# Performance work log

Measured on AMD Instinct MI355X. Metric: run time of the kernel, lower is better.

The kernel has to match this reference:

```python
import jax, jax.numpy as jnp
import numpy as np

N = 100000
E = 1600000
F_FEAT, F_COND, F_HID, F_LAT = 128, 32, 128, 64


def setup_inputs() -> dict:
    key = jax.random.key(0)
    ks = jax.random.split(key, 16)
    feature = jax.random.normal(ks[0], (N, F_FEAT), dtype=jnp.float32)
    condition = jax.random.normal(ks[1], (N, F_COND), dtype=jnp.float32)
    edge_index = jax.random.randint(ks[2], (2, E), 0, N, dtype=jnp.int64)

    def glorot(k, fan_in, fan_out):
        s = jnp.sqrt(6.0 / (fan_in + fan_out)).astype(jnp.float32)
        return jax.random.uniform(k, (fan_in, fan_out), jnp.float32, -s, s)

    enc_in = F_FEAT + F_COND   # 160
    dec_in = F_LAT + F_COND    # 96
    return {
        "feature": feature,
        "condition": condition,
        "edge_index": edge_index,
        "W_e1": glorot(ks[3], enc_in, F_HID), "b_e1": jnp.zeros((F_HID,), jnp.float32),
        "W_e2": glorot(ks[4], F_HID, F_HID), "b_e2": jnp.zeros((F_HID,), jnp.float32),
        "W_e3": glorot(ks[5], F_HID, F_LAT), "b_e3": jnp.zeros((F_LAT,), jnp.float32),
        "W_d1": glorot(ks[6], dec_in, F_HID), "b_d1": jnp.zeros((F_HID,), jnp.float32),
        "W_d2": glorot(ks[7], F_HID, F_HID), "b_d2": jnp.zeros((F_HID,), jnp.float32),
        "W_d3": glorot(ks[8], F_HID, F_FEAT), "b_d3": jnp.zeros((F_FEAT,), jnp.float32),
    }


def _gcn_conv(x, W, b, src, dst, dinv):
    # GCNConv with add_self_loops=True, symmetric normalization:
    # out = D^{-1/2} (A + I) D^{-1/2} X W + b
    h = x @ W                                        # [N, out]
    coef = (dinv[src] * dinv[dst])[:, None]          # [E, 1]
    msg = h[src] * coef                              # [E, out]
    agg = jax.ops.segment_sum(msg, dst, num_segments=x.shape[0])
    agg = agg + h * (dinv * dinv)[:, None]           # self-loop term
    return agg + b


def reference(feature, condition, edge_index,
              W_e1, b_e1, W_e2, b_e2, W_e3, b_e3,
              W_d1, b_d1, W_d2, b_d2, W_d3, b_d3):
    src, dst = edge_index[0], edge_index[1]
    n = feature.shape[0]
    # degree with self loops (edge weights = 1)
    deg = jax.ops.segment_sum(jnp.ones((src.shape[0],), jnp.float32), dst,
                              num_segments=n) + 1.0
    dinv = jax.lax.rsqrt(deg)

    # encoder
    x = jnp.concatenate([feature, condition], axis=1)
    h = jnp.tanh(_gcn_conv(x, W_e1, b_e1, src, dst, dinv))
    h = jnp.tanh(_gcn_conv(h, W_e2, b_e2, src, dst, dinv))
    z = _gcn_conv(h, W_e3, b_e3, src, dst, dinv)

    # decoder
    x = jnp.concatenate([z, condition], axis=1)
    h = jnp.tanh(_gcn_conv(x, W_d1, b_d1, src, dst, dinv))
    h = jnp.tanh(_gcn_conv(h, W_d2, b_d2, src, dst, dinv))
    out = _gcn_conv(h, W_d3, b_d3, src, dst, dinv)
    return out
```

## Files before the change

kernel.cpp:

```cpp
#include <hip/hip_runtime.h>
#include <hip/hip_fp16.h>
#include <math.h>

#define NN 100000
#define NE 1600000
#define NB ((NN + 255) >> 8)
#define CHUNK 8192
#define CAP 8192

typedef __attribute__((ext_vector_type(4))) float floatx4;
typedef __attribute__((ext_vector_type(8))) short shortx8;


__global__ __launch_bounds__(256)
void coarse_hist(const int* __restrict__ ei, int* __restrict__ bucket_cnt, int E) {
    __shared__ int h[512];
    int t = threadIdx.x;
    for (int i = t; i < 512; i += 256) h[i] = 0;
    __syncthreads();
    int base = blockIdx.x * CHUNK;
    int lim = min(base + CHUNK, E);
    for (int e = base + t; e < lim; e += 256) {
        int d = ei[E + e];
        atomicAdd(&h[d >> 8], 1);
    }
    __syncthreads();
    for (int i = t; i < 512; i += 256)
        if (h[i]) atomicAdd(&bucket_cnt[i], h[i]);
}

__global__ void scan_buckets(const int* __restrict__ bucket_cnt,
                             int* __restrict__ bucket_base,
                             int* __restrict__ bucket_fill) {
    __shared__ int sh[512];
    int t = threadIdx.x;
    int v = (t < NB) ? bucket_cnt[t] : 0;
    sh[t] = v;
    __syncthreads();
    for (int off = 1; off < 512; off <<= 1) {
        int u = (t >= off) ? sh[t - off] : 0;
        __syncthreads();
        sh[t] += u;
        __syncthreads();
    }
    int ex = (t == 0) ? 0 : sh[t - 1];
    if (t <= NB) bucket_base[t] = ex;
    if (t < NB) bucket_fill[t] = ex;
}

__global__ __launch_bounds__(256)
void coarse_scatter(const int* __restrict__ ei, int* __restrict__ bucket_fill,
                    unsigned long long* __restrict__ pairs, int E) {
    __shared__ int h[512];
    __shared__ int base[512];
    int t = threadIdx.x;
    for (int i = t; i < 512; i += 256) h[i] = 0;
    __syncthreads();
    int cbase = blockIdx.x * CHUNK;
    int lim = min(cbase + CHUNK, E);
    for (int e = cbase + t; e < lim; e += 256) {
        int d = ei[E + e];
        atomicAdd(&h[d >> 8], 1);
    }
    __syncthreads();
    for (int i = t; i < 512; i += 256)
        base[i] = h[i] ? atomicAdd(&bucket_fill[i], h[i]) : 0;
    __syncthreads();
    for (int i = t; i < 512; i += 256) h[i] = 0;
    __syncthreads();
    for (int e = cbase + t; e < lim; e += 256) {
        int s = ei[e];
        int d = ei[E + e];
        int b = d >> 8;
        int r = atomicAdd(&h[b], 1);
        pairs[base[b] + r] =
            ((unsigned long long)(unsigned)d << 32) | (unsigned)s;
    }
}

__global__ __launch_bounds__(256)
void fine_csr(const unsigned long long* __restrict__ pairs,
              const int* __restrict__ bucket_base,
              int* __restrict__ rowptr, int* __restrict__ colid,
              float* __restrict__ dinv, int n) {
    __shared__ int hist[256];
    __shared__ int offs[256];
    __shared__ int rank[256];
    __shared__ int lbuf[CAP];
    int b = blockIdx.x, t = threadIdx.x;
    int beg = bucket_base[b], end = bucket_base[b + 1];
    int cnt = end - beg;
    hist[t] = 0; rank[t] = 0;
    __syncthreads();
    for (int i = t; i < cnt; i += 256) {
        int d = (int)(pairs[beg + i] >> 32);
        atomicAdd(&hist[d & 255], 1);
    }
    __syncthreads();
    int v = hist[t];
    offs[t] = v;
    __syncthreads();
    for (int off = 1; off < 256; off <<= 1) {
        int u = (t >= off) ? offs[t - off] : 0;
        __syncthreads();
        offs[t] += u;
        __syncthreads();
    }
    int ex = (t == 0) ? 0 : offs[t - 1];
    int node = (b << 8) + t;
    if (node < n) {
        rowptr[node] = beg + ex;
        dinv[node] = rsqrtf((float)v + 1.0f);
    } else if (node == n) {
        rowptr[n] = beg + ex;
    }
    __syncthreads();
    offs[t] = ex;
    __syncthreads();
    for (int i = t; i < cnt; i += 256) {
        unsigned long long p = pairs[beg + i];
        int d = (int)(p >> 32) & 255;
        int s = (int)(p & 0xffffffffu);
        int r = atomicAdd(&rank[d], 1);
        lbuf[offs[d] + r] = s;
    }
    __syncthreads();
    for (int i = t; i < cnt; i += 256) colid[beg + i] = lbuf[i];
}


__device__ __forceinline__ void wsplit_one(const float* __restrict__ W,
                                           unsigned short* __restrict__ Wsw,
                                           int i, int K, int OUT) {
    int k = i / OUT, o = i % OUT;
    float w = W[i];
    unsigned u = __float_as_uint(w);
    float r = w - __uint_as_float(u & 0xFFFF0000u);
    int NT = OUT >> 4;
    int ktc = k >> 5, q = (k >> 3) & 3, j = k & 7;
    int nt = o >> 4, mm = o & 15;
    int lane = (q << 4) | mm;
    size_t base = ((((size_t)(ktc * NT + nt) * 2) * 64 + lane) << 3) + j;
    Wsw[base] = (unsigned short)(u >> 16);
    Wsw[base + 512] = (unsigned short)(__float_as_uint(r) >> 16);
}

__global__ __launch_bounds__(256)
void wsplit_all(const float* __restrict__ W0, unsigned short* __restrict__ O0,
                const float* __restrict__ W1, unsigned short* __restrict__ O1,
                const float* __restrict__ W2, unsigned short* __restrict__ O2,
                const float* __restrict__ W3, unsigned short* __restrict__ O3,
                const float* __restrict__ W4, unsigned short* __restrict__ O4,
                const float* __restrict__ W5, unsigned short* __restrict__ O5) {
    int i = blockIdx.x * 256 + threadIdx.x;
    if (i < 20480) { wsplit_one(W0, O0, i, 160, 128); return; }
    i -= 20480;
    if (i < 16384) { wsplit_one(W1, O1, i, 128, 128); return; }
    i -= 16384;
    if (i < 8192)  { wsplit_one(W2, O2, i, 128, 64);  return; }
    i -= 8192;
    if (i < 12288) { wsplit_one(W3, O3, i, 96, 128);  return; }
    i -= 12288;
    if (i < 16384) { wsplit_one(W4, O4, i, 128, 128); return; }
    i -= 16384;
    if (i < 16384) { wsplit_one(W5, O5, i, 128, 128); }
}


__device__ __forceinline__ void split8(const float* v, shortx8& hi, shortx8& lo) {
#pragma unroll
    for (int i = 0; i < 8; i++) {
        unsigned u = __float_as_uint(v[i]);
        float r = v[i] - __uint_as_float(u & 0xFFFF0000u);
        hi[i] = (short)(u >> 16);
        lo[i] = (short)(__float_as_uint(r) >> 16);
    }
}

template <int OUT, int K, int K1>
__global__ __launch_bounds__(512, 4)
void gemm_mfma(const float* __restrict__ X1, const float* __restrict__ X2,
               const unsigned short* __restrict__ Wsw,
               const float* __restrict__ dinv,
               __half* __restrict__ Y, int ntiles) {
    constexpr int NT = OUT / 16;
    constexpr int NKTC = K / 32;
    constexpr int K2 = K - K1;
    constexpr int PERC = OUT * 128;
    constexpr int CSZ = (65536 / PERC < NKTC) ? (65536 / PERC) : NKTC;
    __shared__ __align__(16) unsigned short lds[CSZ * PERC / 2];

    const int t = threadIdx.x;
    const int wave = t >> 6, lane = t & 63;
    const int m = lane & 15, q = lane >> 4;
    const int tile0 = blockIdx.x * 16 + wave * 2;
    const int tile1 = tile0 + 1;
    const bool act0 = tile0 < ntiles;
    const bool act1 = tile1 < ntiles;
    const int r0 = act0 ? tile0 * 16 + m : 0;
    const int r1 = act1 ? tile1 * 16 + m : 0;
    const float* ap1a = X1 + (size_t)r0 * K1 + q * 8;
    const float* ap1b = X1 + (size_t)r1 * K1 + q * 8;
    const float* ap2a = (K2 > 0) ? (X2 + (size_t)r0 * K2 + q * 8) : X1;
    const float* ap2b = (K2 > 0) ? (X2 + (size_t)r1 * K2 + q * 8) : X1;

    floatx4 acc0[NT], acc1[NT];
#pragma unroll
    for (int nt = 0; nt < NT; nt++) {
        acc0[nt] = (floatx4){0.f, 0.f, 0.f, 0.f};
        acc1[nt] = (floatx4){0.f, 0.f, 0.f, 0.f};
    }

#pragma unroll
    for (int c0 = 0; c0 < NKTC; c0 += CSZ) {
        const int cl = (NKTC - c0 < CSZ) ? (NKTC - c0) : CSZ;
        if (c0 != 0) __syncthreads();
        {
            const float4* gs = (const float4*)Wsw + (size_t)c0 * (PERC / 16);
            float4* ld = (float4*)lds;
            int tot = cl * (PERC / 16);
            for (int i = t; i < tot; i += 512) ld[i] = gs[i];
        }
        __syncthreads();
#pragma unroll
        for (int ktc = 0; ktc < cl; ktc++) {
            const int kg = (c0 + ktc) * 32;
            const float* pa = (kg < K1) ? (ap1a + kg) : (ap2a + (kg - K1));
            const float* pb = (kg < K1) ? (ap1b + kg) : (ap2b + (kg - K1));
            float av0[8], av1[8];
            *(float4*)&av0[0] = *(const float4*)(pa);
            *(float4*)&av0[4] = *(const float4*)(pa + 4);
            *(float4*)&av1[0] = *(const float4*)(pb);
            *(float4*)&av1[4] = *(const float4*)(pb + 4);
            shortx8 ahi0, alo0, ahi1, alo1;
            split8(av0, ahi0, alo0);
            split8(av1, ahi1, alo1);
#pragma unroll
            for (int nt = 0; nt < NT; nt++) {
                const unsigned short* fb =
                    lds + ((((ktc * NT + nt) * 2) * 64 + lane) << 3);
                shortx8 bhi = *(const shortx8*)fb;
                shortx8 blo = *(const shortx8*)(fb + 512);
                acc0[nt] = __builtin_amdgcn_mfma_f32_16x16x32_bf16(ahi0, bhi, acc0[nt], 0, 0, 0);
                acc1[nt] = __builtin_amdgcn_mfma_f32_16x16x32_bf16(ahi1, bhi, acc1[nt], 0, 0, 0);
                acc0[nt] = __builtin_amdgcn_mfma_f32_16x16x32_bf16(ahi0, blo, acc0[nt], 0, 0, 0);
                acc1[nt] = __builtin_amdgcn_mfma_f32_16x16x32_bf16(ahi1, blo, acc1[nt], 0, 0, 0);
                acc0[nt] = __builtin_amdgcn_mfma_f32_16x16x32_bf16(alo0, bhi, acc0[nt], 0, 0, 0);
                acc1[nt] = __builtin_amdgcn_mfma_f32_16x16x32_bf16(alo1, bhi, acc1[nt], 0, 0, 0);
            }
        }
    }

    if (act0) {
        float di[4];
#pragma unroll
        for (int r = 0; r < 4; r++) di[r] = dinv[tile0 * 16 + q * 4 + r];
#pragma unroll
        for (int nt = 0; nt < NT; nt++)
#pragma unroll
            for (int r = 0; r < 4; r++) {
                int orow = tile0 * 16 + q * 4 + r;
                Y[(size_t)orow * OUT + nt * 16 + m] =
                    __float2half_rn(acc0[nt][r] * di[r]);
            }
    }
    if (act1) {
        float di[4];
#pragma unroll
        for (int r = 0; r < 4; r++) di[r] = dinv[tile1 * 16 + q * 4 + r];
#pragma unroll
        for (int nt = 0; nt < NT; nt++)
#pragma unroll
            for (int r = 0; r < 4; r++) {
                int orow = tile1 * 16 + q * 4 + r;
                Y[(size_t)orow * OUT + nt * 16 + m] =
                    __float2half_rn(acc1[nt][r] * di[r]);
            }
    }
}


template <int INW, int OUT, bool CC, bool TANH>
__global__ __launch_bounds__(256, 4)
void fused_pg(const __half2* __restrict__ hin, const float* __restrict__ dinv,
              const int* __restrict__ rowptr, const int* __restrict__ colid,
              const float* __restrict__ biasIn, const float* __restrict__ cond,
              const unsigned short* __restrict__ Wsw,
              __half* __restrict__ hout, int n) {
    constexpr int KG = CC ? INW + 32 : INW;
    constexpr int NT = OUT / 16;
    constexpr int NTW = NT / 4;
    constexpr int NKTC = KG / 32;
    constexpr int LPR = INW / 4;
    constexpr int G = 64 / LPR;
    constexpr int RS2 = INW / 4;

    __shared__ __align__(16) unsigned char xlds[8192];

    const int t = threadIdx.x;
    const int wave = t >> 6, lane = t & 63;
    const int blk = blockIdx.x;
    const int g = lane / LPR, fq = lane % LPR;
    const float2* __restrict__ b2 = (const float2*)hin;

    for (int nd = 0; nd < 4; nd++) {
        int node = blk * 16 + wave * 4 + nd;
        int beg = rowptr[node], end = rowptr[node + 1];
        float ax = 0.f, ay = 0.f, az = 0.f, aw = 0.f;
        int e = beg;
        for (; e + 8 * G <= end; e += 8 * G) {
            int s[8];
#pragma unroll
            for (int j = 0; j < 8; j++) s[j] = colid[e + j * G + g];
            float2 v[8];
#pragma unroll
            for (int j = 0; j < 8; j++) v[j] = b2[(size_t)s[j] * RS2 + fq];
#pragma unroll
            for (int j = 0; j < 8; j++) {
                float2 f0 = __half22float2(*(const __half2*)&v[j].x);
                float2 f1 = __half22float2(*(const __half2*)&v[j].y);
                ax += f0.x; ay += f0.y; az += f1.x; aw += f1.y;
            }
        }
        if (e + 4 * G <= end) {
            int s[4];
#pragma unroll
            for (int j = 0; j < 4; j++) s[j] = colid[e + j * G + g];
            float2 v[4];
#pragma unroll
            for (int j = 0; j < 4; j++) v[j] = b2[(size_t)s[j] * RS2 + fq];
#pragma unroll
            for (int j = 0; j < 4; j++) {
                float2 f0 = __half22float2(*(const __half2*)&v[j].x);
                float2 f1 = __half22float2(*(const __half2*)&v[j].y);
                ax += f0.x; ay += f0.y; az += f1.x; aw += f1.y;
            }
            e += 4 * G;
        }
        for (; e + G <= end; e += G) {
            int s = colid[e + g];
            float2 v = b2[(size_t)s * RS2 + fq];
            float2 f0 = __half22float2(*(const __half2*)&v.x);
            float2 f1 = __half22float2(*(const __half2*)&v.y);
            ax += f0.x; ay += f0.y; az += f1.x; aw += f1.y;
        }
        if (e + g < end) {
            int s = colid[e + g];
            float2 v = b2[(size_t)s * RS2 + fq];
            float2 f0 = __half22float2(*(const __half2*)&v.x);
            float2 f1 = __half22float2(*(const __half2*)&v.y);
            ax += f0.x; ay += f0.y; az += f1.x; aw += f1.y;
        }
        if constexpr (G >= 2) {
            ax += __shfl_xor(ax, LPR); ay += __shfl_xor(ay, LPR);
            az += __shfl_xor(az, LPR); aw += __shfl_xor(aw, LPR);
        }
        if constexpr (G == 4) {
            ax += __shfl_xor(ax, 2 * LPR); ay += __shfl_xor(ay, 2 * LPR);
            az += __shfl_xor(az, 2 * LPR); aw += __shfl_xor(aw, 2 * LPR);
        }
        const int r = wave * 4 + nd;
        if (g == 0) {
            float2 sv = b2[(size_t)node * RS2 + fq];
            float2 f0 = __half22float2(*(const __half2*)&sv.x);
            float2 f1 = __half22float2(*(const __half2*)&sv.y);
            ax += f0.x; ay += f0.y; az += f1.x; aw += f1.y;
            float di = dinv[node];
            float4 bb = *(const float4*)(biasIn + fq * 4);
            float o0 = di * ax + bb.x;
            float o1 = di * ay + bb.y;
            float o2 = di * az + bb.z;
            float o3 = di * aw + bb.w;
            if (TANH) { o0 = tanhf(o0); o1 = tanhf(o1); o2 = tanhf(o2); o3 = tanhf(o3); }
            float o[4] = {o0, o1, o2, o3};
            unsigned short hi[4], lo[4];
#pragma unroll
            for (int i = 0; i < 4; i++) {
                unsigned u = __float_as_uint(o[i]);
                float rr = o[i] - __uint_as_float(u & 0xFFFF0000u);
                hi[i] = (unsigned short)(u >> 16);
                lo[i] = (unsigned short)(__float_as_uint(rr) >> 16);
            }
            int off = (r * 256 + fq * 8) ^ ((r & 7) << 4);
            *(uint2*)(xlds + off) = *(const uint2*)hi;
            *(uint2*)(xlds + 4096 + off) = *(const uint2*)lo;
        }
        if constexpr (CC) {
            if (g == 1 && fq < 8) {
                float4 cv = ((const float4*)cond)[(size_t)node * 8 + fq];
                float c[4] = {cv.x, cv.y, cv.z, cv.w};
                unsigned short hi[4], lo[4];
#pragma unroll
                for (int i = 0; i < 4; i++) {
                    unsigned u = __float_as_uint(c[i]);
                    float rr = c[i] - __uint_as_float(u & 0xFFFF0000u);
                    hi[i] = (unsigned short)(u >> 16);
                    lo[i] = (unsigned short)(__float_as_uint(rr) >> 16);
                }
                int off = (r * 256 + 128 + fq * 8) ^ ((r & 7) << 4);
                *(uint2*)(xlds + off) = *(const uint2*)hi;
                *(uint2*)(xlds + 4096 + off) = *(const uint2*)lo;
            }
        }
    }
    __syncthreads();

    const int m = lane & 15, q = lane >> 4;
    floatx4 acc[NTW];
#pragma unroll
    for (int j = 0; j < NTW; j++) acc[j] = (floatx4){0.f, 0.f, 0.f, 0.f};

#pragma unroll
    for (int kc = 0; kc < NKTC; kc++) {
        int rdoff = (m * 256 + kc * 64 + q * 16) ^ ((m & 7) << 4);
        shortx8 ahi = *(const shortx8*)(xlds + rdoff);
        shortx8 alo = *(const shortx8*)(xlds + 4096 + rdoff);
#pragma unroll
        for (int j = 0; j < NTW; j++) {
            int nt = wave * NTW + j;
            const unsigned short* wp =
                Wsw + ((((size_t)(kc * NT + nt) * 2) * 64 + lane) << 3);
            shortx8 whi = *(const shortx8*)wp;
            shortx8 wlo = *(const shortx8*)(wp + 512);
            acc[j] = __builtin_amdgcn_mfma_f32_16x16x32_bf16(ahi, whi, acc[j], 0, 0, 0);
            acc[j] = __builtin_amdgcn_mfma_f32_16x16x32_bf16(ahi, wlo, acc[j], 0, 0, 0);
            acc[j] = __builtin_amdgcn_mfma_f32_16x16x32_bf16(alo, whi, acc[j], 0, 0, 0);
        }
    }

    float di[4];
#pragma unroll
    for (int r = 0; r < 4; r++) di[r] = dinv[blk * 16 + q * 4 + r];
#pragma unroll
    for (int j = 0; j < NTW; j++) {
        int nt = wave * NTW + j;
#pragma unroll
        for (int r = 0; r < 4; r++) {
            int orow = blk * 16 + q * 4 + r;
            hout[(size_t)orow * OUT + nt * 16 + m] =
                __float2half_rn(acc[j][r] * di[r]);
        }
    }
}


template <int OUT, bool TANH>
__global__ __launch_bounds__(256)
void prop_row(const __half2* __restrict__ hs, const float* __restrict__ dinv,
              const int* __restrict__ rowptr, const int* __restrict__ colid,
              const float* __restrict__ bias, float* __restrict__ out,
              int ldo, int n) {
    constexpr int LPR = OUT / 4;
    constexpr int G = 64 / LPR;
    constexpr int RS2 = OUT / 4;

    int wave = threadIdx.x >> 6, lane = threadIdx.x & 63;
    int node = blockIdx.x * 4 + wave;
    if (node >= n) return;
    int g = lane / LPR, fq = lane % LPR;
    int beg = rowptr[node], end = rowptr[node + 1];
    const float2* __restrict__ b2 = (const float2*)hs;

    float ax = 0.f, ay = 0.f, az = 0.f, aw = 0.f;
    int e = beg;
    for (; e + 8 * G <= end; e += 8 * G) {
        int s[8];
#pragma unroll
        for (int j = 0; j < 8; j++) s[j] = colid[e + j * G + g];
        float2 v[8];
#pragma unroll
        for (int j = 0; j < 8; j++) v[j] = b2[(size_t)s[j] * RS2 + fq];
#pragma unroll
        for (int j = 0; j < 8; j++) {
            float2 f0 = __half22float2(*(const __half2*)&v[j].x);
            float2 f1 = __half22float2(*(const __half2*)&v[j].y);
            ax += f0.x; ay += f0.y; az += f1.x; aw += f1.y;
        }
    }
    if (e + 4 * G <= end) {
        int s[4];
#pragma unroll
        for (int j = 0; j < 4; j++) s[j] = colid[e + j * G + g];
        float2 v[4];
#pragma unroll
        for (int j = 0; j < 4; j++) v[j] = b2[(size_t)s[j] * RS2 + fq];
#pragma unroll
        for (int j = 0; j < 4; j++) {
            float2 f0 = __half22float2(*(const __half2*)&v[j].x);
            float2 f1 = __half22float2(*(const __half2*)&v[j].y);
            ax += f0.x; ay += f0.y; az += f1.x; aw += f1.y;
        }
        e += 4 * G;
    }
    for (; e + G <= end; e += G) {
        int s = colid[e + g];
        float2 v = b2[(size_t)s * RS2 + fq];
        float2 f0 = __half22float2(*(const __half2*)&v.x);
        float2 f1 = __half22float2(*(const __half2*)&v.y);
        ax += f0.x; ay += f0.y; az += f1.x; aw += f1.y;
    }
    if (e + g < end) {
        int s = colid[e + g];
        float2 v = b2[(size_t)s * RS2 + fq];
        float2 f0 = __half22float2(*(const __half2*)&v.x);
        float2 f1 = __half22float2(*(const __half2*)&v.y);
        ax += f0.x; ay += f0.y; az += f1.x; aw += f1.y;
    }

    if constexpr (G >= 2) {
        ax += __shfl_xor(ax, LPR); ay += __shfl_xor(ay, LPR);
        az += __shfl_xor(az, LPR); aw += __shfl_xor(aw, LPR);
    }
    if constexpr (G == 4) {
        ax += __shfl_xor(ax, 2 * LPR); ay += __shfl_xor(ay, 2 * LPR);
        az += __shfl_xor(az, 2 * LPR); aw += __shfl_xor(aw, 2 * LPR);
    }

    if (g == 0) {
        float2 sv = b2[(size_t)node * RS2 + fq];
        float2 f0 = __half22float2(*(const __half2*)&sv.x);
        float2 f1 = __half22float2(*(const __half2*)&sv.y);
        ax += f0.x; ay += f0.y; az += f1.x; aw += f1.y;
        float di = dinv[node];
        float4 bb = *(const float4*)(bias + fq * 4);
        float ox = di * ax + bb.x;
        float oy = di * ay + bb.y;
        float oz = di * az + bb.z;
        float ow = di * aw + bb.w;
        if (TANH) { ox = tanhf(ox); oy = tanhf(oy); oz = tanhf(oz); ow = tanhf(ow); }
        *(float4*)(out + (size_t)node * ldo + fq * 4) = make_float4(ox, oy, oz, ow);
    }
}


extern "C" void kernel_launch(void* const* d_in, const int* in_sizes, int n_in,
                              void* d_out, int out_size, void* d_ws, size_t ws_size,
                              hipStream_t stream) {
    const int n = NN, E = NE;
    const float* feature   = (const float*)d_in[0];
    const float* condition = (const float*)d_in[1];
    const int*   ei        = (const int*)d_in[2];
    const float* W_e1 = (const float*)d_in[3];  const float* b_e1 = (const float*)d_in[4];
    const float* W_e2 = (const float*)d_in[5];  const float* b_e2 = (const float*)d_in[6];
    const float* W_e3 = (const float*)d_in[7];  const float* b_e3 = (const float*)d_in[8];
    const float* W_d1 = (const float*)d_in[9];  const float* b_d1 = (const float*)d_in[10];
    const float* W_d2 = (const float*)d_in[11]; const float* b_d2 = (const float*)d_in[12];
    const float* W_d3 = (const float*)d_in[13]; const float* b_d3 = (const float*)d_in[14];
    float* out = (float*)d_out;

    float*  A    = (float*)d_ws;
    __half* H16a = (__half*)(A + (size_t)n * 160);
    __half* H16b = (__half*)A;
    float*  dinv = (float*)(H16a + (size_t)n * 128);
    int* rowptr  = (int*)(dinv + n);
    int* colid   = rowptr + n + 1;
    uintptr_t pp = (uintptr_t)(colid + E);
    pp = (pp + 15) & ~(uintptr_t)15;
    unsigned long long* pairs = (unsigned long long*)pp;
    int* bucket_cnt  = (int*)(pairs + E);
    int* bucket_base = bucket_cnt + 512;
    int* bucket_fill = bucket_base + 512;
    uintptr_t wp = (uintptr_t)(bucket_fill + 512);
    wp = (wp + 15) & ~(uintptr_t)15;
    unsigned short* wt = (unsigned short*)wp;
    unsigned short* e1w = wt;              unsigned short* e2w = e1w + 160 * 128 * 2;
    unsigned short* e3w = e2w + 128*128*2; unsigned short* d1w = e3w + 128 * 64 * 2;
    unsigned short* d2w = d1w + 96*128*2;  unsigned short* d3w = d2w + 128 * 128 * 2;

    hipMemsetAsync(bucket_cnt, 0, 512 * sizeof(int), stream);

    int nbc = (E + CHUNK - 1) / CHUNK;
    coarse_hist<<<nbc, 256, 0, stream>>>(ei, bucket_cnt, E);
    scan_buckets<<<1, 512, 0, stream>>>(bucket_cnt, bucket_base, bucket_fill);
    coarse_scatter<<<nbc, 256, 0, stream>>>(ei, bucket_fill, pairs, E);
    fine_csr<<<NB, 256, 0, stream>>>(pairs, bucket_base, rowptr, colid, dinv, n);

    wsplit_all<<<(90112 + 255) / 256, 256, 0, stream>>>(
        W_e1, e1w, W_e2, e2w, W_e3, e3w, W_d1, d1w, W_d2, d2w, W_d3, d3w);

    const int ntiles = n / 16;
    const int gb = (ntiles + 15) / 16;
    const int fb = ntiles;
    const int pb = (n + 3) / 4;

    gemm_mfma<128, 160, 128><<<gb, 512, 0, stream>>>(feature, condition, e1w, dinv, H16a, ntiles);
    fused_pg<128, 128, false, true><<<fb, 256, 0, stream>>>(
        (const __half2*)H16a, dinv, rowptr, colid, b_e1, nullptr, e2w, H16b, n);
    fused_pg<128, 64, false, true><<<fb, 256, 0, stream>>>(
        (const __half2*)H16b, dinv, rowptr, colid, b_e2, nullptr, e3w, H16a, n);
    fused_pg<64, 128, true, false><<<fb, 256, 0, stream>>>(
        (const __half2*)H16a, dinv, rowptr, colid, b_e3, condition, d1w, H16b, n);
    fused_pg<128, 128, false, true><<<fb, 256, 0, stream>>>(
        (const __half2*)H16b, dinv, rowptr, colid, b_d1, nullptr, d2w, H16a, n);
    fused_pg<128, 128, false, true><<<fb, 256, 0, stream>>>(
        (const __half2*)H16a, dinv, rowptr, colid, b_d2, nullptr, d3w, H16b, n);
    prop_row<128, false><<<pb, 256, 0, stream>>>(
        (const __half2*)H16b, dinv, rowptr, colid, b_d3, out, 128, n);
}
```

Baseline: 669.4 us.

## Process 32 rows per block in fused propagate-GEMM to reuse weight loads

The fused propagate+GEMM kernel now gathers 32 nodes per block (8 per wave) instead of 16 and runs two 16-row MFMA tiles per weight fragment. Each weight fragment loaded from global memory therefore feeds twice as many MFMAs, halving weight traffic per row. The LDS buffer doubles to 16 KB, the occupancy hint is dropped from launch bounds, and the grid halves. Fewer blocks and more registers may reduce latency hiding for the gather phase. The grid is n/32, which relies on N being divisible by 32 (100000 is).

Result: slower. 723.2 us (+8.0%).

```diff
diff --git a/kernel.cpp b/kernel.cpp
--- a/kernel.cpp
+++ b/kernel.cpp
@@ -281,7 +281,7 @@
 
 
 template <int INW, int OUT, bool CC, bool TANH>
-__global__ __launch_bounds__(256, 4)
+__global__ __launch_bounds__(256)
 void fused_pg(const __half2* __restrict__ hin, const float* __restrict__ dinv,
               const int* __restrict__ rowptr, const int* __restrict__ colid,
               const float* __restrict__ biasIn, const float* __restrict__ cond,
@@ -289,13 +289,13 @@
               __half* __restrict__ hout, int n) {
     constexpr int KG = CC ? INW + 32 : INW;
     constexpr int NT = OUT / 16;
-    constexpr int NTW = NT / 4;
+    constexpr int NPW = NT / 4;
     constexpr int NKTC = KG / 32;
     constexpr int LPR = INW / 4;
     constexpr int G = 64 / LPR;
     constexpr int RS2 = INW / 4;
 
-    __shared__ __align__(16) unsigned char xlds[8192];
+    __shared__ __align__(16) unsigned char xlds[16384];
 
     const int t = threadIdx.x;
     const int wave = t >> 6, lane = t & 63;
@@ -303,8 +303,9 @@
     const int g = lane / LPR, fq = lane % LPR;
     const float2* __restrict__ b2 = (const float2*)hin;
 
-    for (int nd = 0; nd < 4; nd++) {
-        int node = blk * 16 + wave * 4 + nd;
+    for (int nd = 0; nd < 8; nd++) {
+        const int r = wave * 8 + nd;
+        int node = blk * 32 + r;
         int beg = rowptr[node], end = rowptr[node + 1];
         float ax = 0.f, ay = 0.f, az = 0.f, aw = 0.f;
         int e = beg;
@@ -359,7 +360,6 @@
             ax += __shfl_xor(ax, 2 * LPR); ay += __shfl_xor(ay, 2 * LPR);
             az += __shfl_xor(az, 2 * LPR); aw += __shfl_xor(aw, 2 * LPR);
         }
-        const int r = wave * 4 + nd;
         if (g == 0) {
             float2 sv = b2[(size_t)node * RS2 + fq];
             float2 f0 = __half22float2(*(const __half2*)&sv.x);
@@ -383,7 +383,7 @@
             }
             int off = (r * 256 + fq * 8) ^ ((r & 7) << 4);
             *(uint2*)(xlds + off) = *(const uint2*)hi;
-            *(uint2*)(xlds + 4096 + off) = *(const uint2*)lo;
+            *(uint2*)(xlds + 8192 + off) = *(const uint2*)lo;
         }
         if constexpr (CC) {
             if (g == 1 && fq < 8) {
@@ -399,46 +399,60 @@
                 }
                 int off = (r * 256 + 128 + fq * 8) ^ ((r & 7) << 4);
                 *(uint2*)(xlds + off) = *(const uint2*)hi;
-                *(uint2*)(xlds + 4096 + off) = *(const uint2*)lo;
+                *(uint2*)(xlds + 8192 + off) = *(const uint2*)lo;
             }
         }
     }
     __syncthreads();
 
     const int m = lane & 15, q = lane >> 4;
-    floatx4 acc[NTW];
-#pragma unroll
-    for (int j = 0; j < NTW; j++) acc[j] = (floatx4){0.f, 0.f, 0.f, 0.f};
+    floatx4 acc[NPW][2];
+#pragma unroll
+    for (int j = 0; j < NPW; j++) {
+        acc[j][0] = (floatx4){0.f, 0.f, 0.f, 0.f};
+        acc[j][1] = (floatx4){0.f, 0.f, 0.f, 0.f};
+    }
 
 #pragma unroll
     for (int kc = 0; kc < NKTC; kc++) {
-        int rdoff = (m * 256 + kc * 64 + q * 16) ^ ((m & 7) << 4);
-        shortx8 ahi = *(const shortx8*)(xlds + rdoff);
-        shortx8 alo = *(const shortx8*)(xlds + 4096 + rdoff);
-#pragma unroll
-        for (int j = 0; j < NTW; j++) {
-            int nt = wave * NTW + j;
+        int rd0 = (m * 256 + kc * 64 + q * 16) ^ ((m & 7) << 4);
+        int m2 = m + 16;
+        int rd1 = (m2 * 256 + kc * 64 + q * 16) ^ ((m2 & 7) << 4);
+        shortx8 ahi0 = *(const shortx8*)(xlds + rd0);
+        shortx8 alo0 = *(const shortx8*)(xlds + 8192 + rd0);
+        shortx8 ahi1 = *(const shortx8*)(xlds + rd1);
+        shortx8 alo1 = *(const shortx8*)(xlds + 8192 + rd1);
+#pragma unroll
+        for (int j = 0; j < NPW; j++) {
+            int nt = wave + j * 4;
             const unsigned short* wp =
                 Wsw + ((((size_t)(kc * NT + nt) * 2) * 64 + lane) << 3);
             shortx8 whi = *(const shortx8*)wp;
             shortx8 wlo = *(const shortx8*)(wp + 512);
-            acc[j] = __builtin_amdgcn_mfma_f32_16x16x32_bf16(ahi, whi, acc[j], 0, 0, 0);
-            acc[j] = __builtin_amdgcn_mfma_f32_16x16x32_bf16(ahi, wlo, acc[j], 0, 0, 0);
-            acc[j] = __builtin_amdgcn_mfma_f32_16x16x32_bf16(alo, whi, acc[j], 0, 0, 0);
-        }
-    }
-
-    float di[4];
-#pragma unroll
-    for (int r = 0; r < 4; r++) di[r] = dinv[blk * 16 + q * 4 + r];
-#pragma unroll
-    for (int j = 0; j < NTW; j++) {
-        int nt = wave * NTW + j;
-#pragma unroll
-        for (int r = 0; r < 4; r++) {
-            int orow = blk * 16 + q * 4 + r;
-            hout[(size_t)orow * OUT + nt * 16 + m] =
-                __float2half_rn(acc[j][r] * di[r]);
+            acc[j][0] = __builtin_amdgcn_mfma_f32_16x16x32_bf16(ahi0, whi, acc[j][0], 0, 0, 0);
+            acc[j][1] = __builtin_amdgcn_mfma_f32_16x16x32_bf16(ahi1, whi, acc[j][1], 0, 0, 0);
+            acc[j][0] = __builtin_amdgcn_mfma_f32_16x16x32_bf16(ahi0, wlo, acc[j][0], 0, 0, 0);
+            acc[j][1] = __builtin_amdgcn_mfma_f32_16x16x32_bf16(ahi1, wlo, acc[j][1], 0, 0, 0);
+            acc[j][0] = __builtin_amdgcn_mfma_f32_16x16x32_bf16(alo0, whi, acc[j][0], 0, 0, 0);
+            acc[j][1] = __builtin_amdgcn_mfma_f32_16x16x32_bf16(alo1, whi, acc[j][1], 0, 0, 0);
+        }
+    }
+
+#pragma unroll
+    for (int rt = 0; rt < 2; rt++) {
+        float di[4];
+#pragma unroll
+        for (int rr = 0; rr < 4; rr++)
+            di[rr] = dinv[blk * 32 + rt * 16 + q * 4 + rr];
+#pragma unroll
+        for (int j = 0; j < NPW; j++) {
+            int nt = wave + j * 4;
+#pragma unroll
+            for (int rr = 0; rr < 4; rr++) {
+                int orow = blk * 32 + rt * 16 + q * 4 + rr;
+                hout[(size_t)orow * OUT + nt * 16 + m] =
+                    __float2half_rn(acc[j][rt][rr] * di[rr]);
+            }
         }
     }
 }
@@ -580,7 +594,7 @@
 
     const int ntiles = n / 16;
     const int gb = (ntiles + 15) / 16;
-    const int fb = ntiles;
+    const int fb = n / 32;
     const int pb = (n + 3) / 4;
 
     gemm_mfma<128, 160, 128><<<gb, 512, 0, stream>>>(feature, condition, e1w, dinv, H16a, ntiles);
```
